# Kernel optimization log

Hardware: AMD Instinct MI355X
Metric: run time of the kernel (lower is better)

The kernel has to match this reference:

```python
import jax, jax.numpy as jnp
import numpy as np

N = 6            # ensemble members (must match share_mode '6-1')
IN_C = 128
OUT_C = 128
K = 3
STRIDE = 1
PAD = 1
D = IN_C * OUT_C * K * K  # 147456
TEMP = 1.0
ZP1 = 1.2
ZP2 = -0.2
RES_DENOS = (3.0, 5.0)   # res_denos[:maxBWPow] with bw=2 -> [2**2-1, 2**2+1]


def round_ste(v):
    # straight-through round: forward round, backward identity
    return v + jax.lax.stop_gradient(jnp.round(v) - v)


def setup_inputs() -> dict:
    key = jax.random.key(0)
    k1, k2, k3, k4 = jax.random.split(key, 4)
    x = jax.random.normal(k1, (48, IN_C, 64, 64), jnp.float32)
    U = jax.random.normal(k2, (N, D), jnp.float32)
    bp = jax.random.normal(k3, (N + 1, D), jnp.float32)
    # uniform noise for the gumbel-sigmoid sample (open interval to avoid log(0))
    u = jax.random.uniform(k4, (N + 1, D), jnp.float32, 1e-6, 1.0 - 1e-6)
    return {"x": x, "U": U, "bp": bp, "u": u}


def reference(x, U, bp, u):
    beta = jnp.max(U)
    alpha = jnp.min(U)

    # gumbel-sigmoid gating
    g = jnp.log(u / (1.0 - u))
    bsamples = jax.nn.sigmoid((g + bp) / TEMP)
    gates = jnp.clip(bsamples * (ZP1 - ZP2) + ZP2, 0.0, 1.0)  # (7, D)
    # first 6 rows: per-member gates for level 0; last row shared across members for level 1
    gates = jnp.stack([gates[:N], jnp.broadcast_to(gates[N:], (N, D))], axis=0)  # (2, N, D)
    order_gates = jax.lax.stop_gradient(
        jnp.cumprod((gates > 0).astype(gates.dtype), axis=0)
    )

    # sequential residual-bit STE quantization (2 levels)
    s1 = (beta - alpha) / RES_DENOS[0]
    v1 = s1 * round_ste(U / s1)                       # (N, D)
    s2 = s1 / RES_DENOS[1]
    v2 = s2 * round_ste((U - v1.mean(0)) / s2)        # (N, D); vals.sum(0).mean(0) == v1.mean(0)
    vals = jnp.stack([v1, v2], axis=0)                # (2, N, D)

    w = (vals * (gates * order_gates)).sum(0)         # (N, D)
    w = w.reshape(OUT_C * N, IN_C, K, K)

    B = x.shape[0]
    xr = x.reshape(B // N, N * x.shape[1], x.shape[2], x.shape[3])
    act = jax.lax.conv_general_dilated(
        xr, w,
        window_strides=(STRIDE, STRIDE),
        padding=[(PAD, PAD), (PAD, PAD)],
        dimension_numbers=('NCHW', 'OIHW', 'NCHW'),
        feature_group_count=N,
    )
    return act.reshape(act.shape[0] * N, act.shape[1] // N, act.shape[2], act.shape[3])
```

## Files before the change

kernel.cpp:

```cpp
#include <hip/hip_runtime.h>
#include <stdint.h>

typedef __attribute__((ext_vector_type(8))) short bf16x8;
typedef __attribute__((ext_vector_type(4))) float f32x4;

#define DW 147456
#define NTOT (6 * DW)

__device__ __forceinline__ unsigned short f2bf(float f) {
    unsigned int u = __float_as_uint(f);
    u = (u + 0x7FFFu + ((u >> 16) & 1u)) >> 16;
    return (unsigned short)u;
}

__global__ __launch_bounds__(256) void reduce_part(const float* __restrict__ U,
                                                   float* __restrict__ part) {
    int tid = threadIdx.x;
    float mx = -INFINITY, mn = INFINITY;
    const float4* U4 = (const float4*)U;
    for (int i = blockIdx.x * 256 + tid; i < NTOT / 4; i += 256 * 256) {
        float4 v = U4[i];
        mx = fmaxf(fmaxf(fmaxf(mx, v.x), v.y), fmaxf(v.z, v.w));
        mn = fminf(fminf(fminf(mn, v.x), v.y), fminf(v.z, v.w));
    }
    __shared__ float smx[256], smn[256];
    smx[tid] = mx; smn[tid] = mn;
    __syncthreads();
    for (int s = 128; s > 0; s >>= 1) {
        if (tid < s) {
            smx[tid] = fmaxf(smx[tid], smx[tid + s]);
            smn[tid] = fminf(smn[tid], smn[tid + s]);
        }
        __syncthreads();
    }
    if (tid == 0) { part[blockIdx.x] = smx[0]; part[256 + blockIdx.x] = smn[0]; }
}

__global__ __launch_bounds__(256) void make_weights(const float* __restrict__ U,
                                                    const float* __restrict__ bp,
                                                    const float* __restrict__ uu,
                                                    const float* __restrict__ part,
                                                    unsigned short* __restrict__ Wb2) {
    int tid = threadIdx.x;
    __shared__ float smx[256], smn[256];
    smx[tid] = part[tid]; smn[tid] = part[256 + tid];
    __syncthreads();
    for (int s = 128; s > 0; s >>= 1) {
        if (tid < s) {
            smx[tid] = fmaxf(smx[tid], smx[tid + s]);
            smn[tid] = fminf(smn[tid], smn[tid + s]);
        }
        __syncthreads();
    }
    float beta = smx[0], alpha = smn[0];
    float s1 = (beta - alpha) / 3.0f;
    float s2 = s1 / 5.0f;

    int d = blockIdx.x * 256 + tid;

    float v1[6]; float Uv[6]; float vsum = 0.f;
    #pragma unroll
    for (int n = 0; n < 6; n++) {
        float Un = U[n * DW + d];
        Uv[n] = Un;
        float v = s1 * rintf(Un / s1);
        v1[n] = v; vsum += v;
    }
    float vmean = vsum / 6.0f;

    float g6;
    {
        float un = uu[6 * DW + d];
        float sg = un / (un + (1.0f - un) * expf(-bp[6 * DW + d]));
        g6 = fminf(fmaxf(sg * 1.4f - 0.2f, 0.0f), 1.0f);
    }

    int oc = d / 1152;
    int rem = d - oc * 1152;
    int ic = rem / 9;
    int t9 = rem - ic * 9;
    int c = ic >> 5, icc = ic & 31;
    size_t base = ((size_t)c * 9 + t9) * 4096 + (size_t)oc * 32 + icc;

    #pragma unroll
    for (int n = 0; n < 6; n++) {
        float un = uu[n * DW + d];
        float sg = un / (un + (1.0f - un) * expf(-bp[n * DW + d]));
        float g0 = fminf(fmaxf(sg * 1.4f - 0.2f, 0.0f), 1.0f);
        float v2 = s2 * rintf((Uv[n] - vmean) / s2);
        float w = v1[n] * g0 + ((g0 > 0.0f && g6 > 0.0f) ? v2 * g6 : 0.0f);
        Wb2[(size_t)n * DW + base] = f2bf(w);
    }
}

__global__ __launch_bounds__(256) void transform_x(const float* __restrict__ x,
                                                   unsigned short* __restrict__ xT) {
    __shared__ unsigned short Sh[128 * 70];
    int b = blockIdx.x;
    int img = b >> 6, row = b & 63;
    int tid = threadIdx.x;
    {
        int ch = tid >> 1;
        int col0 = (tid & 1) * 32;
        const float* src = x + (((size_t)(img * 128 + ch) * 64 + row) * 64 + col0);
        #pragma unroll
        for (int j = 0; j < 8; j++) {
            float4 v = ((const float4*)src)[j];
            unsigned int p0 = (unsigned int)f2bf(v.x) | ((unsigned int)f2bf(v.y) << 16);
            unsigned int p1 = (unsigned int)f2bf(v.z) | ((unsigned int)f2bf(v.w) << 16);
            unsigned int* dst = (unsigned int*)&Sh[ch * 70 + col0 + j * 4];
            dst[0] = p0; dst[1] = p1;
        }
    }
    __syncthreads();
    {
        int col = tid & 63;
        int q = tid >> 6;
        int chg = q * 32;
        union { unsigned short s[32]; uint4 v[4]; } tmp;
        #pragma unroll
        for (int j = 0; j < 32; j++) tmp.s[j] = Sh[(chg + j) * 70 + col];
        uint4* dst = (uint4*)(xT + ((size_t)img * 524288 + (size_t)q * 131072 +
                                    (size_t)row * 2048 + col * 32));
        #pragma unroll
        for (int k = 0; k < 4; k++) dst[k] = tmp.v[k];
    }
}

typedef const __attribute__((address_space(1))) void CGV;
typedef __attribute__((address_space(3))) void LV;

__global__ __launch_bounds__(256) void conv_mfma(const unsigned short* __restrict__ xT,
                                                 const unsigned short* __restrict__ Wb2,
                                                 float* __restrict__ out) {
    __shared__ __align__(16) unsigned short Xs[6 * 66 * 32];
    __shared__ __align__(16) unsigned short Ws[9 * 64 * 32];
    int blk = blockIdx.x;
    int band = blk & 15;
    int och = (blk >> 4) & 1;
    int img = blk >> 5;
    int row0 = band * 4;
    int mem = img - (img / 6) * 6;
    const unsigned short* Wsrc = Wb2 + (size_t)mem * DW + och * 2048;
    const unsigned short* Xsrc = xT + (size_t)img * 524288;

    int tid = threadIdx.x;
    int lane = tid & 63;
    int prow = tid >> 6;
    int lr = lane & 15, lq = lane >> 4;

    if (tid < 192) {
        int r = tid >> 5, j = tid & 31;
        int col = (j < 16) ? 0 : 65;
        *(unsigned int*)&Xs[(r * 66 + col) * 32 + (j & 15) * 2] = 0u;
    }

    auto stage = [&](int c) {
        #pragma unroll
        for (int t = 0; t < 9; t++)
            __builtin_amdgcn_global_load_lds((CGV*)(Wsrc + (c * 9 + t) * 4096 + tid * 8),
                                             (LV*)(&Ws[t * 2048 + tid * 8]), 16, 0, 0);
        #pragma unroll
        for (int r = 0; r < 6; r++) {
            int srow = row0 + r - 1;
            if ((unsigned)srow < 64u)
                __builtin_amdgcn_global_load_lds((CGV*)(Xsrc + c * 131072 + srow * 2048 + tid * 8),
                                                 (LV*)(&Xs[(r * 66 + 1) * 32 + tid * 8]), 16, 0, 0);
            else
                *(uint4*)&Xs[(r * 66 + 1) * 32 + tid * 8] = make_uint4(0u, 0u, 0u, 0u);
        }
    };

    f32x4 acc[4][4];
    #pragma unroll
    for (int mi = 0; mi < 4; mi++)
        #pragma unroll
        for (int ni = 0; ni < 4; ni++)
            acc[mi][ni] = (f32x4){0.f, 0.f, 0.f, 0.f};

    stage(0);
    __syncthreads();

    for (int c = 0; c < 4; c++) {
        #pragma unroll
        for (int t = 0; t < 9; t++) {
            int dy = t / 3, dx = t - dy * 3;
            bf16x8 af[4], bfr[4];
            #pragma unroll
            for (int mi = 0; mi < 4; mi++)
                af[mi] = *(const bf16x8*)(&Ws[t * 2048 + (mi * 16 + lr) * 32 + lq * 8]);
            #pragma unroll
            for (int ni = 0; ni < 4; ni++)
                bfr[ni] = *(const bf16x8*)(&Xs[((prow + dy) * 66 + ni * 16 + lr + dx) * 32 + lq * 8]);
            #pragma unroll
            for (int mi = 0; mi < 4; mi++)
                #pragma unroll
                for (int ni = 0; ni < 4; ni++)
                    acc[mi][ni] = __builtin_amdgcn_mfma_f32_16x16x32_bf16(
                        af[mi], bfr[ni], acc[mi][ni], 0, 0, 0);
        }
        if (c < 3) {
            __syncthreads();
            stage(c + 1);
            __syncthreads();
        }
    }

    float* obase = out + (size_t)img * 524288 + (size_t)(row0 + prow) * 64;
    #pragma unroll
    for (int mi = 0; mi < 4; mi++) {
        #pragma unroll
        for (int ni = 0; ni < 4; ni++) {
            int px = ni * 16 + lr;
            int ocb = och * 64 + mi * 16 + lq * 4;
            #pragma unroll
            for (int rr = 0; rr < 4; rr++)
                obase[(size_t)(ocb + rr) * 4096 + px] = acc[mi][ni][rr];
        }
    }
}

extern "C" void kernel_launch(void* const* d_in, const int* in_sizes, int n_in,
                              void* d_out, int out_size, void* d_ws, size_t ws_size,
                              hipStream_t stream) {
    const float* x  = (const float*)d_in[0];
    const float* U  = (const float*)d_in[1];
    const float* bp = (const float*)d_in[2];
    const float* uu = (const float*)d_in[3];
    float* out = (float*)d_out;

    char* ws = (char*)d_ws;
    float* part = (float*)ws;
    unsigned short* Wb2 = (unsigned short*)(ws + 4096);
    unsigned short* xT  = (unsigned short*)(ws + 4096 + 1769472);

    reduce_part <<<256, 256, 0, stream>>>(U, part);
    make_weights<<<576, 256, 0, stream>>>(U, bp, uu, part, Wb2);
    transform_x <<<48 * 64, 256, 0, stream>>>(x, xT);
    conv_mfma   <<<48 * 32, 256, 0, stream>>>(xT, Wb2, out);
}
```

Measured before the change: 252.9 us.

## Enlarge conv tile to 8 rows, swizzle LDS layouts, remap block order

The conv kernel now computes 8 output rows per block instead of 4, so each wave holds a 4x8 accumulator tile. This halves the block count and reuses each staged weight tile across twice as many pixels. Weights are pre-laid out in MFMA-fragment order so LDS reads are contiguous per lane. The x transform applies an XOR swizzle on 16-byte chunks that the conv reads undo, aimed at avoiding LDS bank conflicts. Blocks are reordered across the grid and launch bounds request 2 blocks per CU, which raises register pressure from the doubled accumulators.

```diff
diff --git a/kernel.cpp b/kernel.cpp
--- a/kernel.cpp
+++ b/kernel.cpp
@@ -80,7 +80,11 @@
     int ic = rem / 9;
     int t9 = rem - ic * 9;
     int c = ic >> 5, icc = ic & 31;
-    size_t base = ((size_t)c * 9 + t9) * 4096 + (size_t)oc * 32 + icc;
+    int och = oc >> 6, ocl = oc & 63;
+    int mi = ocl >> 4, lrr = ocl & 15;
+    int lq = icc >> 3, jj = icc & 7;
+    size_t base = ((size_t)(c * 2 + och) * 9 + t9) * 2048
+                + (size_t)mi * 512 + (size_t)(lq * 16 + lrr) * 8 + jj;
 
     #pragma unroll
     for (int n = 0; n < 6; n++) {
@@ -117,51 +121,57 @@
         int col = tid & 63;
         int q = tid >> 6;
         int chg = q * 32;
+        int h = ((col + 1) >> 1) & 3;
         union { unsigned short s[32]; uint4 v[4]; } tmp;
         #pragma unroll
         for (int j = 0; j < 32; j++) tmp.s[j] = Sh[(chg + j) * 70 + col];
         uint4* dst = (uint4*)(xT + ((size_t)img * 524288 + (size_t)q * 131072 +
                                     (size_t)row * 2048 + col * 32));
         #pragma unroll
-        for (int k = 0; k < 4; k++) dst[k] = tmp.v[k];
+        for (int k = 0; k < 4; k++) dst[k] = tmp.v[k ^ h];
     }
 }
 
 typedef const __attribute__((address_space(1))) void CGV;
 typedef __attribute__((address_space(3))) void LV;
 
-__global__ __launch_bounds__(256) void conv_mfma(const unsigned short* __restrict__ xT,
-                                                 const unsigned short* __restrict__ Wb2,
-                                                 float* __restrict__ out) {
-    __shared__ __align__(16) unsigned short Xs[6 * 66 * 32];
+__global__ __launch_bounds__(256, 2) void conv_mfma(const unsigned short* __restrict__ xT,
+                                                    const unsigned short* __restrict__ Wb2,
+                                                    float* __restrict__ out) {
+    __shared__ __align__(16) unsigned short Xs[10 * 66 * 32];
     __shared__ __align__(16) unsigned short Ws[9 * 64 * 32];
-    int blk = blockIdx.x;
-    int band = blk & 15;
-    int och = (blk >> 4) & 1;
-    int img = blk >> 5;
-    int row0 = band * 4;
+    int o = blockIdx.x;
+    int blk = (o & 7) * 96 + (o >> 3);
+    int band = blk & 7;
+    int och = (blk >> 3) & 1;
+    int img = blk >> 4;
+    int row0 = band * 8;
     int mem = img - (img / 6) * 6;
-    const unsigned short* Wsrc = Wb2 + (size_t)mem * DW + och * 2048;
+    const unsigned short* Wmem = Wb2 + (size_t)mem * DW;
     const unsigned short* Xsrc = xT + (size_t)img * 524288;
 
     int tid = threadIdx.x;
     int lane = tid & 63;
-    int prow = tid >> 6;
+    int w = tid >> 6;
     int lr = lane & 15, lq = lane >> 4;
-
-    if (tid < 192) {
-        int r = tid >> 5, j = tid & 31;
+    int so0 = (lq ^ ((lr >> 1) & 3)) * 8;
+    int so1 = (lq ^ (((lr + 1) >> 1) & 3)) * 8;
+    int so2 = (lq ^ (((lr + 2) >> 1) & 3)) * 8;
+
+    for (int i = tid; i < 320; i += 256) {
+        int r = i >> 5, j = i & 31;
         int col = (j < 16) ? 0 : 65;
         *(unsigned int*)&Xs[(r * 66 + col) * 32 + (j & 15) * 2] = 0u;
     }
 
     auto stage = [&](int c) {
+        const unsigned short* wsrc = Wmem + (size_t)((c * 2 + och) * 9) * 2048;
         #pragma unroll
         for (int t = 0; t < 9; t++)
-            __builtin_amdgcn_global_load_lds((CGV*)(Wsrc + (c * 9 + t) * 4096 + tid * 8),
+            __builtin_amdgcn_global_load_lds((CGV*)(wsrc + t * 2048 + tid * 8),
                                              (LV*)(&Ws[t * 2048 + tid * 8]), 16, 0, 0);
         #pragma unroll
-        for (int r = 0; r < 6; r++) {
+        for (int r = 0; r < 10; r++) {
             int srow = row0 + r - 1;
             if ((unsigned)srow < 64u)
                 __builtin_amdgcn_global_load_lds((CGV*)(Xsrc + c * 131072 + srow * 2048 + tid * 8),
@@ -171,11 +181,11 @@
         }
     };
 
-    f32x4 acc[4][4];
+    f32x4 acc[4][8];
     #pragma unroll
     for (int mi = 0; mi < 4; mi++)
         #pragma unroll
-        for (int ni = 0; ni < 4; ni++)
+        for (int ni = 0; ni < 8; ni++)
             acc[mi][ni] = (f32x4){0.f, 0.f, 0.f, 0.f};
 
     stage(0);
@@ -184,18 +194,22 @@
     for (int c = 0; c < 4; c++) {
         #pragma unroll
         for (int t = 0; t < 9; t++) {
-            int dy = t / 3, dx = t - dy * 3;
-            bf16x8 af[4], bfr[4];
+            const int dy = t / 3, dx = t - (t / 3) * 3;
+            const int so = (dx == 0) ? so0 : (dx == 1) ? so1 : so2;
+            bf16x8 af[4], bfr[8];
             #pragma unroll
             for (int mi = 0; mi < 4; mi++)
-                af[mi] = *(const bf16x8*)(&Ws[t * 2048 + (mi * 16 + lr) * 32 + lq * 8]);
-            #pragma unroll
-            for (int ni = 0; ni < 4; ni++)
-                bfr[ni] = *(const bf16x8*)(&Xs[((prow + dy) * 66 + ni * 16 + lr + dx) * 32 + lq * 8]);
+                af[mi] = *(const bf16x8*)(&Ws[t * 2048 + mi * 512 + lane * 8]);
+            #pragma unroll
+            for (int ni = 0; ni < 8; ni++) {
+                int xrow = w * 2 + (ni >> 2) + dy;
+                int col = (ni & 3) * 16 + lr + dx;
+                bfr[ni] = *(const bf16x8*)(&Xs[(xrow * 66 + col) * 32 + so]);
+            }
             #pragma unroll
             for (int mi = 0; mi < 4; mi++)
                 #pragma unroll
-                for (int ni = 0; ni < 4; ni++)
+                for (int ni = 0; ni < 8; ni++)
                     acc[mi][ni] = __builtin_amdgcn_mfma_f32_16x16x32_bf16(
                         af[mi], bfr[ni], acc[mi][ni], 0, 0, 0);
         }
@@ -206,16 +220,17 @@
         }
     }
 
-    float* obase = out + (size_t)img * 524288 + (size_t)(row0 + prow) * 64;
+    float* obase = out + (size_t)img * 524288;
     #pragma unroll
     for (int mi = 0; mi < 4; mi++) {
         #pragma unroll
-        for (int ni = 0; ni < 4; ni++) {
-            int px = ni * 16 + lr;
+        for (int ni = 0; ni < 8; ni++) {
+            int r = row0 + w * 2 + (ni >> 2);
+            int px = (ni & 3) * 16 + lr;
             int ocb = och * 64 + mi * 16 + lq * 4;
             #pragma unroll
             for (int rr = 0; rr < 4; rr++)
-                obase[(size_t)(ocb + rr) * 4096 + px] = acc[mi][ni][rr];
+                obase[(size_t)(ocb + rr) * 4096 + (size_t)r * 64 + px] = acc[mi][ni][rr];
         }
     }
 }
@@ -237,5 +252,5 @@
     reduce_part <<<256, 256, 0, stream>>>(U, part);
     make_weights<<<576, 256, 0, stream>>>(U, bp, uu, part, Wb2);
     transform_x <<<48 * 64, 256, 0, stream>>>(x, xT);
-    conv_mfma   <<<48 * 32, 256, 0, stream>>>(xT, Wb2, out);
-}
+    conv_mfma   <<<48 * 16, 256, 0, stream>>>(xT, Wb2, out);
+}
```

After: 286.5 us. 1.13x slower.

## Pre-swizzle weight and activation layouts to remove LDS bank conflicts; remap blocks

Applied to the files above, without the earlier changes.

Changes the weight layout written by make_weights so each MFMA A-fragment becomes one contiguous lane-indexed read of LDS. Applies an XOR swizzle to the 16-byte chunks of each transformed x pixel, with matching swizzled offsets in the conv B-fragment reads, to avoid LDS bank conflicts. Also remaps block indices for better L2 locality and adds a min-2-blocks occupancy hint. The risk is that a mismatch between the swizzle in the producer and consumer would silently corrupt results, and the occupancy hint could cause register spills.

```diff
diff --git a/kernel.cpp b/kernel.cpp
--- a/kernel.cpp
+++ b/kernel.cpp
@@ -80,7 +80,11 @@
     int ic = rem / 9;
     int t9 = rem - ic * 9;
     int c = ic >> 5, icc = ic & 31;
-    size_t base = ((size_t)c * 9 + t9) * 4096 + (size_t)oc * 32 + icc;
+    int och = oc >> 6, ocl = oc & 63;
+    int mi = ocl >> 4, lrr = ocl & 15;
+    int lq = icc >> 3, jj = icc & 7;
+    size_t base = ((size_t)(c * 2 + och) * 9 + t9) * 2048
+                + (size_t)mi * 512 + (size_t)(lq * 16 + lrr) * 8 + jj;
 
     #pragma unroll
     for (int n = 0; n < 6; n++) {
@@ -117,37 +121,42 @@
         int col = tid & 63;
         int q = tid >> 6;
         int chg = q * 32;
+        int h = ((col + 1) >> 1) & 3;
         union { unsigned short s[32]; uint4 v[4]; } tmp;
         #pragma unroll
         for (int j = 0; j < 32; j++) tmp.s[j] = Sh[(chg + j) * 70 + col];
         uint4* dst = (uint4*)(xT + ((size_t)img * 524288 + (size_t)q * 131072 +
                                     (size_t)row * 2048 + col * 32));
         #pragma unroll
-        for (int k = 0; k < 4; k++) dst[k] = tmp.v[k];
+        for (int k = 0; k < 4; k++) dst[k] = tmp.v[k ^ h];
     }
 }
 
 typedef const __attribute__((address_space(1))) void CGV;
 typedef __attribute__((address_space(3))) void LV;
 
-__global__ __launch_bounds__(256) void conv_mfma(const unsigned short* __restrict__ xT,
-                                                 const unsigned short* __restrict__ Wb2,
-                                                 float* __restrict__ out) {
+__global__ __launch_bounds__(256, 2) void conv_mfma(const unsigned short* __restrict__ xT,
+                                                    const unsigned short* __restrict__ Wb2,
+                                                    float* __restrict__ out) {
     __shared__ __align__(16) unsigned short Xs[6 * 66 * 32];
     __shared__ __align__(16) unsigned short Ws[9 * 64 * 32];
-    int blk = blockIdx.x;
+    int o = blockIdx.x;
+    int blk = (o & 7) * 192 + (o >> 3);
     int band = blk & 15;
     int och = (blk >> 4) & 1;
     int img = blk >> 5;
     int row0 = band * 4;
     int mem = img - (img / 6) * 6;
-    const unsigned short* Wsrc = Wb2 + (size_t)mem * DW + och * 2048;
+    const unsigned short* Wmem = Wb2 + (size_t)mem * DW;
     const unsigned short* Xsrc = xT + (size_t)img * 524288;
 
     int tid = threadIdx.x;
     int lane = tid & 63;
     int prow = tid >> 6;
     int lr = lane & 15, lq = lane >> 4;
+    int so0 = (lq ^ ((lr >> 1) & 3)) * 8;
+    int so1 = (lq ^ (((lr + 1) >> 1) & 3)) * 8;
+    int so2 = (lq ^ (((lr + 2) >> 1) & 3)) * 8;
 
     if (tid < 192) {
         int r = tid >> 5, j = tid & 31;
@@ -156,9 +165,10 @@
     }
 
     auto stage = [&](int c) {
+        const unsigned short* wsrc = Wmem + (size_t)((c * 2 + och) * 9) * 2048;
         #pragma unroll
         for (int t = 0; t < 9; t++)
-            __builtin_amdgcn_global_load_lds((CGV*)(Wsrc + (c * 9 + t) * 4096 + tid * 8),
+            __builtin_amdgcn_global_load_lds((CGV*)(wsrc + t * 2048 + tid * 8),
                                              (LV*)(&Ws[t * 2048 + tid * 8]), 16, 0, 0);
         #pragma unroll
         for (int r = 0; r < 6; r++) {
@@ -184,14 +194,17 @@
     for (int c = 0; c < 4; c++) {
         #pragma unroll
         for (int t = 0; t < 9; t++) {
-            int dy = t / 3, dx = t - dy * 3;
+            const int dy = t / 3, dx = t - (t / 3) * 3;
+            const int so = (dx == 0) ? so0 : (dx == 1) ? so1 : so2;
             bf16x8 af[4], bfr[4];
             #pragma unroll
             for (int mi = 0; mi < 4; mi++)
-                af[mi] = *(const bf16x8*)(&Ws[t * 2048 + (mi * 16 + lr) * 32 + lq * 8]);
-            #pragma unroll
-            for (int ni = 0; ni < 4; ni++)
-                bfr[ni] = *(const bf16x8*)(&Xs[((prow + dy) * 66 + ni * 16 + lr + dx) * 32 + lq * 8]);
+                af[mi] = *(const bf16x8*)(&Ws[t * 2048 + mi * 512 + lane * 8]);
+            #pragma unroll
+            for (int ni = 0; ni < 4; ni++) {
+                int col = ni * 16 + lr + dx;
+                bfr[ni] = *(const bf16x8*)(&Xs[((prow + dy) * 66 + col) * 32 + so]);
+            }
             #pragma unroll
             for (int mi = 0; mi < 4; mi++)
                 #pragma unroll
```

Result: slower. 266.5 us (+5.4%).
